# Performance work log

Measured on AMD Instinct MI355X. Metric: run time of the kernel, lower is better.

## Reference

```python
import jax, jax.numpy as jnp
import numpy as np

# BiAttn: additive (concat-based) cross attention.
# Original torch: e = Linear([k_i ; q_j]) = k_i @ W[:H] + q_j @ W[H:] + b  (separable)
# a = softmax(e, axis=-1 over Y); out[b,x,h] = sum_y v[b,y,h] * a[b,x,y]

B, X, Y, H = 8, 2048, 2048, 1024


def setup_inputs() -> dict:
    key = jax.random.key(0)
    kq, kk, kv, kw = jax.random.split(key, 4)
    q = jax.random.normal(kq, (B, Y, H), dtype=jnp.float32)
    k = jax.random.normal(kk, (B, X, H), dtype=jnp.float32)
    v = jax.random.normal(kv, (B, Y, H), dtype=jnp.float32)
    W = jax.random.normal(kw, (2 * H,), dtype=jnp.float32) * (1.0 / np.sqrt(2 * H))
    b = jnp.zeros((), dtype=jnp.float32)
    return {"q": q, "k": k, "v": v, "W": W, "b": b}


def reference(q, k, v, W, b):
    Hdim = k.shape[-1]
    Wk, Wq = W[:Hdim], W[Hdim:]
    # Separable additive score: e[b,x,y] = k[b,x]@Wk + q[b,y]@Wq + b
    sk = jnp.einsum('bxh,h->bx', k, Wk)          # [B, X]
    sq = jnp.einsum('byh,h->by', q, Wq)          # [B, Y]
    e = sk[:, :, None] + sq[:, None, :] + b      # [B, X, Y]
    a = jax.nn.softmax(e, axis=-1)               # softmax over Y
    out = jnp.einsum('byh,bxy->bxh', v, a)       # [B, X, H]
    return out
```

## Files before the change

kernel.cpp:

```cpp
#include <hip/hip_runtime.h>

#define Bn 8
#define Xn 2048
#define Yn 2048
#define Hn 1024
#define RPB 8
#define YC 32
#define NCH (Yn / YC)


__global__ __launch_bounds__(256)
void k_pe(const float* __restrict__ q, const float* __restrict__ W,
          float* __restrict__ pe, float* __restrict__ sb) {
    const int blk = blockIdx.x;
    const int t = threadIdx.x;
    const int wave = t >> 6, lane = t & 63;
    __shared__ float ps[RPB];

    const float4* w4 = (const float4*)(W + Hn);
    const float4 ww0 = w4[lane];
    const float4 ww1 = w4[lane + 64];
    const float4 ww2 = w4[lane + 128];
    const float4 ww3 = w4[lane + 192];

    const int ra = blk * RPB + wave * 2;
    const float4* qa = (const float4*)(q + (size_t)ra * Hn);
    const float4* qb = qa + (Hn / 4);
    float acca = 0.f, accb = 0.f;
    #pragma unroll
    for (int i = 0; i < 4; ++i) {
        float4 a  = qa[lane + 64 * i];
        float4 bb = qb[lane + 64 * i];
        float4 w  = (i == 0) ? ww0 : (i == 1) ? ww1 : (i == 2) ? ww2 : ww3;
        acca += a.x * w.x + a.y * w.y + a.z * w.z + a.w * w.w;
        accb += bb.x * w.x + bb.y * w.y + bb.z * w.z + bb.w * w.w;
    }
    #pragma unroll
    for (int off = 32; off > 0; off >>= 1) {
        acca += __shfl_xor(acca, off, 64);
        accb += __shfl_xor(accb, off, 64);
    }
    if (lane == 0) {
        float ea = __expf(acca), eb = __expf(accb);
        pe[ra] = ea; pe[ra + 1] = eb;
        ps[wave * 2] = ea; ps[wave * 2 + 1] = eb;
    }
    __syncthreads();
    if (t == 0) {
        float s = 0.f;
        #pragma unroll
        for (int i = 0; i < RPB; ++i) s += ps[i];
        sb[blk] = s;
    }
}

__global__ __launch_bounds__(256)
void k_pv(const float* __restrict__ v, const float* __restrict__ pe,
          float* __restrict__ o_part) {
    const int b = blockIdx.y;
    const int c = blockIdx.x;
    const int y0 = c * YC;
    const int t = threadIdx.x;
    __shared__ float pw[YC];
    if (t < YC) pw[t] = pe[b * Yn + y0 + t];
    __syncthreads();

    const float4* v4 = (const float4*)(v + ((size_t)b * Yn + y0) * Hn);
    float4 acc = {0.f, 0.f, 0.f, 0.f};
    #pragma unroll 16
    for (int yy = 0; yy < YC; ++yy) {
        const float p = pw[yy];
        const float4 vv = v4[(size_t)yy * (Hn / 4) + t];
        acc.x = fmaf(p, vv.x, acc.x);
        acc.y = fmaf(p, vv.y, acc.y);
        acc.z = fmaf(p, vv.z, acc.z);
        acc.w = fmaf(p, vv.w, acc.w);
    }
    ((float4*)o_part)[((size_t)c * Bn + b) * (Hn / 4) + t] = acc;
}

__global__ __launch_bounds__(256)
void k_red(const float* __restrict__ o_part, const float* __restrict__ sb,
           float* __restrict__ o_final) {
    const int b = blockIdx.x;
    const int t = threadIdx.x;
    const int wave = t >> 6, lane = t & 63;
    __shared__ float wred[4];

    float s = sb[b * (Yn / RPB) + t];
    #pragma unroll
    for (int off = 32; off > 0; off >>= 1) s += __shfl_xor(s, off, 64);
    if (lane == 0) wred[wave] = s;
    __syncthreads();
    const float den = wred[0] + wred[1] + wred[2] + wred[3];
    const float inv = 1.f / den;

    float4 acc = {0.f, 0.f, 0.f, 0.f};
    const float4* op4 = (const float4*)o_part;
    #pragma unroll 8
    for (int c = 0; c < NCH; ++c) {
        const float4 p = op4[((size_t)c * Bn + b) * (Hn / 4) + t];
        acc.x += p.x; acc.y += p.y; acc.z += p.z; acc.w += p.w;
    }
    acc.x *= inv; acc.y *= inv; acc.z *= inv; acc.w *= inv;
    ((float4*)o_final)[b * (Hn / 4) + t] = acc;
}

__global__ void k_bcast(const float* __restrict__ o, float4* __restrict__ out) {
    const size_t i = (size_t)blockIdx.x * blockDim.x + threadIdx.x;
    const int h4 = (int)(i & (Hn / 4 - 1));
    const size_t row = i >> 8;
    const int b = (int)(row >> 11);
    const float4* o4 = (const float4*)o;
    out[i] = o4[b * (Hn / 4) + h4];
}

extern "C" void kernel_launch(void* const* d_in, const int* in_sizes, int n_in,
                              void* d_out, int out_size, void* d_ws, size_t ws_size,
                              hipStream_t stream) {
    const float* q = (const float*)d_in[0];
    const float* v = (const float*)d_in[2];
    const float* W = (const float*)d_in[3];
    float* out = (float*)d_out;

    float* pe     = (float*)d_ws;
    float* sb     = pe + (size_t)Bn * Yn;
    float* o_part = sb + Bn * Yn / RPB;
    float* o_fin  = o_part + (size_t)NCH * Bn * Hn;

    k_pe   <<<Bn * Yn / RPB, 256, 0, stream>>>(q, W, pe, sb);
    k_pv   <<<dim3(NCH, Bn), 256, 0, stream>>>(v, pe, o_part);
    k_red  <<<Bn, 256, 0, stream>>>(o_part, sb, o_fin);
    k_bcast<<<(Bn * (size_t)Xn * Hn / 4) / 256, 256, 0, stream>>>(o_fin, (float4*)out);
}
```

Measured before the change: 209.1 us.

## Fuse partial-sum reduction into PV kernel via atomics and drop reduce kernel

Removes the separate reduction kernel. Each PV block now computes the softmax denominator itself and pre-scales its weights. It then atomically adds its partial output directly into the final vector, which the first kernel zeroes. The Y chunk size is doubled so fewer blocks contend on the atomics. This saves one launch and the partial-buffer round trip, at the cost of float atomics whose summation order is nondeterministic.

```diff
diff --git a/kernel.cpp b/kernel.cpp
--- a/kernel.cpp
+++ b/kernel.cpp
@@ -5,17 +5,21 @@
 #define Yn 2048
 #define Hn 1024
 #define RPB 8
-#define YC 32
+#define NPB (Yn / RPB)
+#define YC 64
 #define NCH (Yn / YC)
 
 
 __global__ __launch_bounds__(256)
 void k_pe(const float* __restrict__ q, const float* __restrict__ W,
-          float* __restrict__ pe, float* __restrict__ sb) {
+          float* __restrict__ pe, float* __restrict__ sb,
+          float* __restrict__ o) {
     const int blk = blockIdx.x;
     const int t = threadIdx.x;
     const int wave = t >> 6, lane = t & 63;
     __shared__ float ps[RPB];
+
+    if (t == 0) ((float4*)o)[blk] = make_float4(0.f, 0.f, 0.f, 0.f);
 
     const float4* w4 = (const float4*)(W + Hn);
     const float4 ww0 = w4[lane];
@@ -56,13 +60,23 @@
 
 __global__ __launch_bounds__(256)
 void k_pv(const float* __restrict__ v, const float* __restrict__ pe,
-          float* __restrict__ o_part) {
+          const float* __restrict__ sb, float* __restrict__ o) {
     const int b = blockIdx.y;
     const int c = blockIdx.x;
     const int y0 = c * YC;
     const int t = threadIdx.x;
+    const int wave = t >> 6, lane = t & 63;
+    __shared__ float wred[4];
     __shared__ float pw[YC];
-    if (t < YC) pw[t] = pe[b * Yn + y0 + t];
+
+    float s = sb[b * NPB + t];
+    #pragma unroll
+    for (int off = 32; off > 0; off >>= 1) s += __shfl_xor(s, off, 64);
+    if (lane == 0) wred[wave] = s;
+    __syncthreads();
+    const float inv = 1.f / (wred[0] + wred[1] + wred[2] + wred[3]);
+
+    if (t < YC) pw[t] = pe[b * Yn + y0 + t] * inv;
     __syncthreads();
 
     const float4* v4 = (const float4*)(v + ((size_t)b * Yn + y0) * Hn);
@@ -76,34 +90,11 @@
         acc.z = fmaf(p, vv.z, acc.z);
         acc.w = fmaf(p, vv.w, acc.w);
     }
-    ((float4*)o_part)[((size_t)c * Bn + b) * (Hn / 4) + t] = acc;
-}
-
-__global__ __launch_bounds__(256)
-void k_red(const float* __restrict__ o_part, const float* __restrict__ sb,
-           float* __restrict__ o_final) {
-    const int b = blockIdx.x;
-    const int t = threadIdx.x;
-    const int wave = t >> 6, lane = t & 63;
-    __shared__ float wred[4];
-
-    float s = sb[b * (Yn / RPB) + t];
-    #pragma unroll
-    for (int off = 32; off > 0; off >>= 1) s += __shfl_xor(s, off, 64);
-    if (lane == 0) wred[wave] = s;
-    __syncthreads();
-    const float den = wred[0] + wred[1] + wred[2] + wred[3];
-    const float inv = 1.f / den;
-
-    float4 acc = {0.f, 0.f, 0.f, 0.f};
-    const float4* op4 = (const float4*)o_part;
-    #pragma unroll 8
-    for (int c = 0; c < NCH; ++c) {
-        const float4 p = op4[((size_t)c * Bn + b) * (Hn / 4) + t];
-        acc.x += p.x; acc.y += p.y; acc.z += p.z; acc.w += p.w;
-    }
-    acc.x *= inv; acc.y *= inv; acc.z *= inv; acc.w *= inv;
-    ((float4*)o_final)[b * (Hn / 4) + t] = acc;
+    float* ob = o + b * Hn + 4 * t;
+    atomicAdd(ob + 0, acc.x);
+    atomicAdd(ob + 1, acc.y);
+    atomicAdd(ob + 2, acc.z);
+    atomicAdd(ob + 3, acc.w);
 }
 
 __global__ void k_bcast(const float* __restrict__ o, float4* __restrict__ out) {
@@ -123,13 +114,11 @@
     const float* W = (const float*)d_in[3];
     float* out = (float*)d_out;
 
-    float* pe     = (float*)d_ws;
-    float* sb     = pe + (size_t)Bn * Yn;
-    float* o_part = sb + Bn * Yn / RPB;
-    float* o_fin  = o_part + (size_t)NCH * Bn * Hn;
+    float* pe = (float*)d_ws;
+    float* sb = pe + (size_t)Bn * Yn;
+    float* o  = sb + Bn * NPB;
 
-    k_pe   <<<Bn * Yn / RPB, 256, 0, stream>>>(q, W, pe, sb);
-    k_pv   <<<dim3(NCH, Bn), 256, 0, stream>>>(v, pe, o_part);
-    k_red  <<<Bn, 256, 0, stream>>>(o_part, sb, o_fin);
-    k_bcast<<<(Bn * (size_t)Xn * Hn / 4) / 256, 256, 0, stream>>>(o_fin, (float4*)out);
+    k_pe   <<<Bn * Yn / RPB, 256, 0, stream>>>(q, W, pe, sb, o);
+    k_pv   <<<dim3(NCH, Bn), 256, 0, stream>>>(v, pe, sb, o);
+    k_bcast<<<(Bn * (size_t)Xn * Hn / 4) / 256, 256, 0, stream>>>(o, (float4*)out);
 }
```

Result: faster. 203.7 us, median of 2 (-2.6%).
